# Optimization experiments

Hardware: AMD Instinct MI355X
Metric: run time of the kernel (lower is better)

## Reference

```python
import jax, jax.numpy as jnp
import numpy as np


def _haar_dwt2(x):
    # x: [b, H, W] -> (ll, lh, hl, hh), each [b, H/2, W/2]; orthonormal 2D Haar
    a = x[:, ::2, ::2]
    b = x[:, ::2, 1::2]
    c = x[:, 1::2, ::2]
    d = x[:, 1::2, 1::2]
    ll = (a + b + c + d) * 0.5
    lh = (a + b - c - d) * 0.5  # detail along rows (frames)
    hl = (a - b + c - d) * 0.5  # detail along cols (features)
    hh = (a - b - c + d) * 0.5
    return ll, lh, hl, hh


def _haar_idwt2(ll, lh, hl, hh):
    a = (ll + lh + hl + hh) * 0.5
    b = (ll + lh - hl - hh) * 0.5
    c = (ll - lh + hl - hh) * 0.5
    d = (ll - lh - hl + hh) * 0.5
    B, H2, W2 = ll.shape
    out = jnp.zeros((B, 2 * H2, 2 * W2), ll.dtype)
    out = out.at[:, ::2, ::2].set(a)
    out = out.at[:, ::2, 1::2].set(b)
    out = out.at[:, 1::2, ::2].set(c)
    out = out.at[:, 1::2, 1::2].set(d)
    return out


def _interp_linear_last(x, m):
    # linear interpolation along last dim from linspace(0,1,n) to linspace(0,1,m)
    n = x.shape[-1]
    pos = jnp.linspace(0.0, 1.0, m, dtype=x.dtype) * (n - 1)
    i0 = jnp.clip(jnp.floor(pos).astype(jnp.int32), 0, n - 2)
    w = pos - i0.astype(x.dtype)
    return x[..., i0] * (1.0 - w) + x[..., i0 + 1] * w


def setup_inputs() -> dict:
    key = jax.random.key(0)
    k0, k1, k2 = jax.random.split(key, 3)
    b, f, c, hidden = 128, 256, 512, 2048
    x = jax.random.normal(k0, (b, f, c), dtype=jnp.float32)
    fc1_w = jax.random.normal(k1, (hidden, c), dtype=jnp.float32) * 0.02
    fc1_b = jnp.zeros((hidden,), dtype=jnp.float32)
    fc2_w = jax.random.normal(k2, (c // 2, hidden), dtype=jnp.float32) * 0.02
    fc2_b = jnp.zeros((c // 2,), dtype=jnp.float32)
    return {"x": x, "fc1_w": fc1_w, "fc1_b": fc1_b, "fc2_w": fc2_w, "fc2_b": fc2_b}


def reference(x, fc1_w, fc1_b, fc2_w, fc2_b):
    b, f, c = x.shape
    ll, lh, hl, hh = _haar_dwt2(x)               # [b, f/2, c/2] each
    ll_up = _interp_linear_last(ll, c)           # [b, f/2, c]
    h = jax.nn.gelu(jnp.einsum('bfc,hc->bfh', ll_up, fc1_w) + fc1_b, approximate=False)
    ll_new = jnp.einsum('bfh,oh->bfo', h, fc2_w) + fc2_b  # [b, f/2, c/2]
    return _haar_idwt2(ll_new, lh, hl, hh)       # [b, f, c]
```

## Files before the change

kernel.cpp:

```cpp
#include <hip/hip_runtime.h>
#include <hip/hip_bf16.h>
#include <stdint.h>

typedef __bf16 bf16;
typedef __attribute__((ext_vector_type(8)))  __bf16 bf16x8;
typedef __attribute__((ext_vector_type(16))) float  f32x16;
typedef __attribute__((ext_vector_type(4)))  float  f32x4v;
typedef __attribute__((ext_vector_type(2)))  float  f32x2v;

#define B_DIM 128
#define F_DIM 256
#define C_DIM 512
#define HID   2048
#define C2    256
#define MROWS 16384

static constexpr size_t OFF_W1 = 0;
static constexpr size_t OFF_W2 = 1u << 20;

__device__ __forceinline__ unsigned short bfbits(float f) {
    bf16 h = (bf16)f;
    return __builtin_bit_cast(unsigned short, h);
}

__global__ __launch_bounds__(256) void prep_kernel(
    const float* __restrict__ w1, const float* __restrict__ w2,
    bf16* __restrict__ w1pp, bf16* __restrict__ w2pp)
{
    const int blk = blockIdx.x;
    const int t = threadIdx.x;
    if (blk < 2048) {
        int idx = blk * 256 + t;
        int h = idx >> 8, k = idx & 255;
        const float* wrow = w1 + (size_t)h * C_DIM;
        float acc = 0.f;
        int jlo = (k == 0) ? 0 : (int)((float)(k - 1) * (511.0f / 255.0f));
        int jhi = (int)((float)(k + 1) * (511.0f / 255.0f)) + 1;
        if (jhi > 511) jhi = 511;
        for (int j = jlo; j <= jhi; ++j) {
            float pos = (float)j * (255.0f / 511.0f);
            int i0 = (int)pos;
            if (i0 > 254) i0 = 254;
            float w = pos - (float)i0;
            float coef = (i0 == k) ? (1.0f - w) : ((i0 + 1 == k) ? w : 0.0f);
            acc += coef * wrow[j];
        }
        size_t frag = (size_t)(h >> 5) * 16 + (k >> 4);
        size_t lane = (size_t)(((k >> 3) & 1) << 5 | (h & 31));
        w1pp[frag * 512 + lane * 8 + (k & 7)] = (bf16)acc;
    } else {
        int idx2 = (blk - 2048) * 256 + t;
        int c2 = idx2 >> 11, hid = idx2 & 2047;
        float v = w2[(size_t)c2 * HID + hid];
        size_t frag = (size_t)(c2 >> 5) * 128 + (hid >> 4);
        size_t lane = (size_t)(((hid >> 3) & 1) << 5 | (c2 & 31));
        w2pp[frag * 512 + lane * 8 + (hid & 7)] = (bf16)v;
    }
}

__global__ __launch_bounds__(512, 4) void fused_mlp(
    const bf16* __restrict__ w1pp, const bf16* __restrict__ w2pp,
    const float* __restrict__ b1, const float* __restrict__ b2,
    const float* __restrict__ x, float* __restrict__ out)
{
    __shared__ __align__(16) char smem[49152];
    char* hsm = smem + 16384;

    const int tid = threadIdx.x;
    const int l   = tid & 63;
    const int wv  = tid >> 6;
    const int sub = wv >> 2;
    const int sl4 = wv & 3;
    const int R0  = blockIdx.x * 32;
    const char* w1B = (const char*)w1pp;
    const char* w2B = (const char*)w2pp;

    bf16x8 wf[4];
    {
        const char* w1f0 = w1B + (size_t)(sub * 8 + sl4 * 2) * 16 * 1024 + (size_t)l * 16;
        wf[0] = *(const bf16x8*)(w1f0);
        wf[1] = *(const bf16x8*)(w1f0 + 16 * 1024);
        wf[2] = *(const bf16x8*)(w1f0 + 1024);
        wf[3] = *(const bf16x8*)(w1f0 + 16 * 1024 + 1024);
    }

    {
        const int r = tid & 31;
        const int s = tid >> 5;
        const int gbf = R0 + r;
        const float* xr0 = x + ((size_t)(gbf >> 7) * F_DIM + (size_t)(gbf & 127) * 2) * C_DIM;
        const float* xr1 = xr0 + C_DIM;
#pragma unroll
        for (int jj = 0; jj < 2; ++jj) {
            int j = s * 2 + jj;
            f32x4v a[4], b[4];
#pragma unroll
            for (int i = 0; i < 4; ++i) {
                a[i] = __builtin_nontemporal_load((const f32x4v*)(xr0 + (j * 4 + i) * 4));
                b[i] = __builtin_nontemporal_load((const f32x4v*)(xr1 + (j * 4 + i) * 4));
            }
            const float* pa = (const float*)a;
            const float* pb = (const float*)b;
            bf16x8 pk;
#pragma unroll
            for (int e = 0; e < 8; ++e)
                pk[e] = (bf16)(0.5f * (pa[2*e] + pa[2*e+1] + pb[2*e] + pb[2*e+1]));
            *(bf16x8*)(smem + s * 1024 + (size_t)((jj << 5) | r) * 16) = pk;
        }
    }
    __syncthreads();

    f32x16 acc2{};

#pragma unroll 1
    for (int pc = 0; pc < 4; ++pc) {
        const char* w1f = w1B + (size_t)(pc * 16 + sub * 8 + sl4 * 2) * 16 * 1024 + (size_t)l * 16;
        const char* w2f = w2B + ((size_t)(wv * 128 + pc * 32)) * 1024 + (size_t)l * 16;
        const int pn = (pc + 1) & 3;
        const char* w1fn = w1B + (size_t)(pn * 16 + sub * 8 + sl4 * 2) * 16 * 1024 + (size_t)l * 16;

        f32x16 acc1_0{}, acc1_1{};
#pragma unroll
        for (int ks = 0; ks < 16; ++ks) {
            bf16x8 af = *(const bf16x8*)(smem + ks * 1024 + (size_t)l * 16);
            acc1_0 = __builtin_amdgcn_mfma_f32_32x32x16_bf16(af, wf[(2 * ks) & 3], acc1_0, 0, 0, 0);
            acc1_1 = __builtin_amdgcn_mfma_f32_32x32x16_bf16(af, wf[(2 * ks + 1) & 3], acc1_1, 0, 0, 0);
            if (ks < 14) {
                wf[(2 * ks) & 3]     = *(const bf16x8*)(w1f + (ks + 2) * 1024);
                wf[(2 * ks + 1) & 3] = *(const bf16x8*)(w1f + 16 * 1024 + (ks + 2) * 1024);
            } else {
                int v0 = (ks - 14) * 2;
                wf[(2 * ks) & 3]     = *(const bf16x8*)(w2f + (v0 + 0) * 1024);
                wf[(2 * ks + 1) & 3] = *(const bf16x8*)(w2f + (v0 + 1) * 1024);
            }
        }

#pragma unroll
        for (int nf = 0; nf < 2; ++nf) {
            const f32x16& A = nf ? acc1_1 : acc1_0;
            const int cin = sub * 256 + sl4 * 64 + nf * 32 + (l & 31);
            const float bs = b1[pc * 512 + cin];
            const int kf2 = cin >> 4;
#pragma unroll
            for (int reg = 0; reg < 16; ++reg) {
                float v = A[reg] + bs;
                float tt = v * (0.79788456080f + 0.03567740814f * v * v);
                float g = v / (1.0f + __expf(-2.0f * tt));
                float gp = __builtin_bit_cast(float,
                    __builtin_amdgcn_mov_dpp(__builtin_bit_cast(int, g), 0xB1, 0xF, 0xF, true));
                if (!(l & 1)) {
                    unsigned u = (unsigned)bfbits(g) | ((unsigned)bfbits(gp) << 16);
                    int crow = (reg & 3) + 8 * (reg >> 2) + 4 * (l >> 5);
                    int lane2 = (((l >> 3) & 1) << 5) | crow;
                    *(unsigned*)(hsm + kf2 * 1024 + lane2 * 16 + (l & 7) * 2) = u;
                }
            }
        }
        __syncthreads();

#pragma unroll
        for (int v = 0; v < 32; ++v) {
            bf16x8 hf = *(const bf16x8*)(hsm + v * 1024 + (size_t)l * 16);
            acc2 = __builtin_amdgcn_mfma_f32_32x32x16_bf16(hf, wf[v & 3], acc2, 0, 0, 0);
            if (v < 28) {
                wf[v & 3] = *(const bf16x8*)(w2f + (v + 4) * 1024);
            } else {
                int u = v - 28;
                wf[v & 3] = *(const bf16x8*)(w1fn + (u & 1) * 16 * 1024 + (u >> 1) * 1024);
            }
        }
        __syncthreads();
    }

    {
        const int c2 = wv * 32 + (l & 31);
        const float bs = b2[c2];
#pragma unroll
        for (int reg = 0; reg < 16; ++reg) {
            int R = R0 + (reg & 3) + 8 * (reg >> 2) + 4 * (l >> 5);
            int b = R >> 7, f2 = R & 127;
            const float* xr = x + ((size_t)b * F_DIM + (size_t)f2 * 2) * C_DIM;
            f32x2v p0 = __builtin_nontemporal_load((const f32x2v*)(xr + c2 * 2));
            f32x2v p1 = __builtin_nontemporal_load((const f32x2v*)(xr + C_DIM + c2 * 2));
            float llo = 0.5f * (p0[0] + p0[1] + p1[0] + p1[1]);
            float d = 0.5f * ((acc2[reg] + bs) - llo);
            f32x2v o0, o1;
            o0[0] = p0[0] + d; o0[1] = p0[1] + d;
            o1[0] = p1[0] + d; o1[1] = p1[1] + d;
            float* orow = out + ((size_t)b * F_DIM + (size_t)f2 * 2) * C_DIM;
            __builtin_nontemporal_store(o0, (f32x2v*)(orow + c2 * 2));
            __builtin_nontemporal_store(o1, (f32x2v*)(orow + C_DIM + c2 * 2));
        }
    }
}

extern "C" void kernel_launch(void* const* d_in, const int* in_sizes, int n_in,
                              void* d_out, int out_size, void* d_ws, size_t ws_size,
                              hipStream_t stream) {
    const float* x     = (const float*)d_in[0];
    const float* fc1_w = (const float*)d_in[1];
    const float* fc1_b = (const float*)d_in[2];
    const float* fc2_w = (const float*)d_in[3];
    const float* fc2_b = (const float*)d_in[4];
    float* out = (float*)d_out;

    char* ws = (char*)d_ws;
    bf16* w1pp = (bf16*)(ws + OFF_W1);
    bf16* w2pp = (bf16*)(ws + OFF_W2);

    prep_kernel<<<4096, 256, 0, stream>>>(fc1_w, fc2_w, w1pp, w2pp);
    fused_mlp<<<MROWS / 32, 512, 0, stream>>>(w1pp, w2pp, fc1_b, fc2_b, x, out);
}
```

Baseline: 110.4 us.

## Stream weight fragments through per-wave LDS ring via global_load_lds

Replaces the register-based prefetch of weight fragments with direct global-to-LDS async loads into a 4-slot per-wave ring buffer, keeping three loads in flight and using manual vmcnt waits and sched barriers. It also hoists bias loads ahead of the loop, fully unrolls the pc loop, and swaps __syncthreads for lgkmcnt waits plus a raw s_barrier. The goal is to hide global load latency behind MFMA work and free VGPRs. In exchange LDS use grows from 48KB to 80KB per block, which may cut occupancy, and it adds an extra LDS read per MFMA.

Measured after the change: 123.9 us. +12.3%, slower.

```diff
diff --git a/kernel.cpp b/kernel.cpp
--- a/kernel.cpp
+++ b/kernel.cpp
@@ -8,7 +8,6 @@
 typedef __attribute__((ext_vector_type(4)))  float  f32x4v;
 typedef __attribute__((ext_vector_type(2)))  float  f32x2v;
 
-#define B_DIM 128
 #define F_DIM 256
 #define C_DIM 512
 #define HID   2048
@@ -22,6 +21,19 @@
     bf16 h = (bf16)f;
     return __builtin_bit_cast(unsigned short, h);
 }
+
+typedef const __attribute__((address_space(1))) unsigned int as1_uint;
+typedef __attribute__((address_space(3))) unsigned int as3_uint;
+__device__ __forceinline__ void gld_lds16(const void* g, void* l) {
+    as1_uint* gp = (as1_uint*)(uintptr_t)g;
+    as3_uint* lp = (as3_uint*)(uintptr_t)l;
+    __builtin_amdgcn_global_load_lds(gp, lp, 16, 0, 0);
+}
+
+#define WAITVM2() asm volatile("s_waitcnt vmcnt(2)" ::: "memory")
+#define WAITVM0() asm volatile("s_waitcnt vmcnt(0)" ::: "memory")
+#define LGKM0()   asm volatile("s_waitcnt lgkmcnt(0)" ::: "memory")
+#define SCHED0()  __builtin_amdgcn_sched_barrier(0)
 
 __global__ __launch_bounds__(256) void prep_kernel(
     const float* __restrict__ w1, const float* __restrict__ w2,
@@ -63,7 +75,7 @@
     const float* __restrict__ b1, const float* __restrict__ b2,
     const float* __restrict__ x, float* __restrict__ out)
 {
-    __shared__ __align__(16) char smem[49152];
+    __shared__ __align__(16) char smem[81920];
     char* hsm = smem + 16384;
 
     const int tid = threadIdx.x;
@@ -72,16 +84,24 @@
     const int sub = wv >> 2;
     const int sl4 = wv & 3;
     const int R0  = blockIdx.x * 32;
+    char* ringb = smem + 49152 + wv * 4096;
+    const size_t loff = (size_t)l * 16;
     const char* w1B = (const char*)w1pp;
     const char* w2B = (const char*)w2pp;
 
-    bf16x8 wf[4];
+    float bs[8];
+#pragma unroll
+    for (int pc = 0; pc < 4; ++pc)
+#pragma unroll
+        for (int nf = 0; nf < 2; ++nf)
+            bs[pc * 2 + nf] = b1[pc * 512 + sub * 256 + sl4 * 64 + nf * 32 + (l & 31)];
+    const float b2v = b2[wv * 32 + (l & 31)];
+
     {
-        const char* w1f0 = w1B + (size_t)(sub * 8 + sl4 * 2) * 16 * 1024 + (size_t)l * 16;
-        wf[0] = *(const bf16x8*)(w1f0);
-        wf[1] = *(const bf16x8*)(w1f0 + 16 * 1024);
-        wf[2] = *(const bf16x8*)(w1f0 + 1024);
-        wf[3] = *(const bf16x8*)(w1f0 + 16 * 1024 + 1024);
+        const char* w1f = w1B + (size_t)(sub * 8 + sl4 * 2) * 16384 + loff;
+        gld_lds16(w1f,          ringb + 0 * 1024 + loff);
+        gld_lds16(w1f + 16384,  ringb + 1 * 1024 + loff);
+        gld_lds16(w1f + 1024,   ringb + 2 * 1024 + loff);
     }
 
     {
@@ -112,38 +132,42 @@
 
     f32x16 acc2{};
 
-#pragma unroll 1
+#pragma unroll
     for (int pc = 0; pc < 4; ++pc) {
-        const char* w1f = w1B + (size_t)(pc * 16 + sub * 8 + sl4 * 2) * 16 * 1024 + (size_t)l * 16;
-        const char* w2f = w2B + ((size_t)(wv * 128 + pc * 32)) * 1024 + (size_t)l * 16;
-        const int pn = (pc + 1) & 3;
-        const char* w1fn = w1B + (size_t)(pn * 16 + sub * 8 + sl4 * 2) * 16 * 1024 + (size_t)l * 16;
+        const char* w1f = w1B + (size_t)(pc * 16 + sub * 8 + sl4 * 2) * 16384 + loff;
+        const char* w2f = w2B + (size_t)(wv * 128 + pc * 32) * 1024 + loff;
+        const char* nx1 = (pc < 3)
+            ? w1B + (size_t)((pc + 1) * 16 + sub * 8 + sl4 * 2) * 16384 + loff
+            : w1B + loff;
 
         f32x16 acc1_0{}, acc1_1{};
-#pragma unroll
-        for (int ks = 0; ks < 16; ++ks) {
-            bf16x8 af = *(const bf16x8*)(smem + ks * 1024 + (size_t)l * 16);
-            acc1_0 = __builtin_amdgcn_mfma_f32_32x32x16_bf16(af, wf[(2 * ks) & 3], acc1_0, 0, 0, 0);
-            acc1_1 = __builtin_amdgcn_mfma_f32_32x32x16_bf16(af, wf[(2 * ks + 1) & 3], acc1_1, 0, 0, 0);
-            if (ks < 14) {
-                wf[(2 * ks) & 3]     = *(const bf16x8*)(w1f + (ks + 2) * 1024);
-                wf[(2 * ks + 1) & 3] = *(const bf16x8*)(w1f + 16 * 1024 + (ks + 2) * 1024);
+        bf16x8 af;
+#pragma unroll
+        for (int u = 0; u < 32; ++u) {
+            WAITVM2();
+            SCHED0();
+            if ((u & 1) == 0)
+                af = *(const bf16x8*)(smem + (u >> 1) * 1024 + loff);
+            bf16x8 wfr = *(const bf16x8*)(ringb + (u & 3) * 1024 + loff);
+            if (u < 29) {
+                gld_lds16(w1f + ((u + 3) & 1) * 16384 + ((u + 3) >> 1) * 1024,
+                          ringb + ((u + 3) & 3) * 1024 + loff);
             } else {
-                int v0 = (ks - 14) * 2;
-                wf[(2 * ks) & 3]     = *(const bf16x8*)(w2f + (v0 + 0) * 1024);
-                wf[(2 * ks + 1) & 3] = *(const bf16x8*)(w2f + (v0 + 1) * 1024);
-            }
+                gld_lds16(w2f + (u - 29) * 1024, ringb + ((u + 3) & 3) * 1024 + loff);
+            }
+            if (u & 1) acc1_1 = __builtin_amdgcn_mfma_f32_32x32x16_bf16(af, wfr, acc1_1, 0, 0, 0);
+            else       acc1_0 = __builtin_amdgcn_mfma_f32_32x32x16_bf16(af, wfr, acc1_0, 0, 0, 0);
         }
 
 #pragma unroll
         for (int nf = 0; nf < 2; ++nf) {
             const f32x16& A = nf ? acc1_1 : acc1_0;
             const int cin = sub * 256 + sl4 * 64 + nf * 32 + (l & 31);
-            const float bs = b1[pc * 512 + cin];
+            const float bsv = bs[pc * 2 + nf];
             const int kf2 = cin >> 4;
 #pragma unroll
             for (int reg = 0; reg < 16; ++reg) {
-                float v = A[reg] + bs;
+                float v = A[reg] + bsv;
                 float tt = v * (0.79788456080f + 0.03567740814f * v * v);
                 float g = v / (1.0f + __expf(-2.0f * tt));
                 float gp = __builtin_bit_cast(float,
@@ -156,25 +180,33 @@
                 }
             }
         }
-        __syncthreads();
+        SCHED0(); LGKM0();
+        __builtin_amdgcn_s_barrier();
+        SCHED0();
 
 #pragma unroll
         for (int v = 0; v < 32; ++v) {
-            bf16x8 hf = *(const bf16x8*)(hsm + v * 1024 + (size_t)l * 16);
-            acc2 = __builtin_amdgcn_mfma_f32_32x32x16_bf16(hf, wf[v & 3], acc2, 0, 0, 0);
-            if (v < 28) {
-                wf[v & 3] = *(const bf16x8*)(w2f + (v + 4) * 1024);
+            WAITVM2();
+            SCHED0();
+            bf16x8 hf  = *(const bf16x8*)(hsm + v * 1024 + loff);
+            bf16x8 wfr = *(const bf16x8*)(ringb + (v & 3) * 1024 + loff);
+            if (v < 29) {
+                gld_lds16(w2f + (v + 3) * 1024, ringb + ((v + 3) & 3) * 1024 + loff);
             } else {
-                int u = v - 28;
-                wf[v & 3] = *(const bf16x8*)(w1fn + (u & 1) * 16 * 1024 + (u >> 1) * 1024);
-            }
-        }
-        __syncthreads();
-    }
+                int u = v - 29;
+                gld_lds16(nx1 + (u & 1) * 16384 + (u >> 1) * 1024,
+                          ringb + ((v + 3) & 3) * 1024 + loff);
+            }
+            acc2 = __builtin_amdgcn_mfma_f32_32x32x16_bf16(hf, wfr, acc2, 0, 0, 0);
+        }
+        SCHED0(); LGKM0();
+        __builtin_amdgcn_s_barrier();
+        SCHED0();
+    }
+    WAITVM0();
 
     {
         const int c2 = wv * 32 + (l & 31);
-        const float bs = b2[c2];
 #pragma unroll
         for (int reg = 0; reg < 16; ++reg) {
             int R = R0 + (reg & 3) + 8 * (reg >> 2) + 4 * (l >> 5);
@@ -183,7 +215,7 @@
             f32x2v p0 = __builtin_nontemporal_load((const f32x2v*)(xr + c2 * 2));
             f32x2v p1 = __builtin_nontemporal_load((const f32x2v*)(xr + C_DIM + c2 * 2));
             float llo = 0.5f * (p0[0] + p0[1] + p1[0] + p1[1]);
-            float d = 0.5f * ((acc2[reg] + bs) - llo);
+            float d = 0.5f * ((acc2[reg] + b2v) - llo);
             f32x2v o0, o1;
             o0[0] = p0[0] + d; o0[1] = p0[1] + d;
             o1[0] = p1[0] + d; o1[1] = p1[1] + d;
```
